# Kernel tuning notes

Measured on AMD Instinct MI355X. Metric: run time of the kernel, lower is better.

Reference implementation:

```python
import jax, jax.numpy as jnp
import numpy as np

N = 100000
E = 1600000
IN_FEATS = 256
HIDDEN = 128
CLASSES = 40

def _glorot(key, fan_in, fan_out):
    lim = float(np.sqrt(6.0 / (fan_in + fan_out)))
    return jax.random.uniform(key, (fan_in, fan_out), jnp.float32, -lim, lim)

def setup_inputs() -> dict:
    key = jax.random.key(0)
    ks = jax.random.split(key, 8)
    x = jax.random.normal(ks[0], (N, IN_FEATS), jnp.float32)
    src = jax.random.randint(ks[1], (E,), 0, N, jnp.int32)
    dst = jax.random.randint(ks[2], (E,), 0, N, jnp.int32)
    W0 = _glorot(ks[3], IN_FEATS, HIDDEN)
    b0 = jnp.zeros((HIDDEN,), jnp.float32)
    W1 = _glorot(ks[4], HIDDEN, HIDDEN)
    b1 = jnp.zeros((HIDDEN,), jnp.float32)
    Wc = _glorot(ks[5], HIDDEN, CLASSES)
    bc = jnp.zeros((CLASSES,), jnp.float32)
    return {"x": x, "src": src, "dst": dst, "W0": W0, "b0": b0,
            "W1": W1, "b1": b1, "Wc": Wc, "bc": bc}

def _degree_norms(src, dst, n):
    ones = jnp.ones(src.shape[0], jnp.float32)
    out_deg = jax.ops.segment_sum(ones, src, num_segments=n)
    in_deg = jax.ops.segment_sum(ones, dst, num_segments=n)
    c_src = jax.lax.rsqrt(jnp.maximum(out_deg, 1.0))  # D_out^{-1/2}
    c_dst = jax.lax.rsqrt(jnp.maximum(in_deg, 1.0))   # D_in^{-1/2}
    return c_src, c_dst

def _graph_conv(h, src, dst, c_src, c_dst, W, b, n):
    # transform first (cheaper when widths shrink), math-equivalent to DGL norm='both'
    h = h @ W
    h = h * c_src[:, None]
    agg = jax.ops.segment_sum(h[src], dst, num_segments=n)  # spmm gather/scatter
    return agg * c_dst[:, None] + b

def reference(x, src, dst, W0, b0, W1, b1, Wc, bc):
    n = x.shape[0]
    c_src, c_dst = _degree_norms(src, dst, n)
    h = _graph_conv(x, src, dst, c_src, c_dst, W0, b0, n)
    h = jax.nn.relu(h)  # dropout is identity at eval
    h = _graph_conv(h, src, dst, c_src, c_dst, W1, b1, n)
    logits = jax.nn.relu(h) @ Wc + bc
    return (h, logits)
```

## Files before the change

kernel.cpp:

```cpp
#include <hip/hip_runtime.h>
#include <cstdint>
#include <cstddef>


#define NPB 128
#define BSHIFT 7
#define NBLK_E 256

typedef __attribute__((ext_vector_type(8))) short short8;
typedef __attribute__((ext_vector_type(4))) float f32x4;

static __device__ __forceinline__ float4 ld4(const float* p) { return *(const float4*)p; }

static __device__ __forceinline__ float bf2f(unsigned int u) {
  union { unsigned int i; float f; } x; x.i = u << 16; return x.f;
}
static __device__ __forceinline__ unsigned int f2bf(float f) {
  union { float f; unsigned int i; } x; x.f = f;
  unsigned int r = x.i + 0x7fff + ((x.i >> 16) & 1);
  return r >> 16;
}

__global__ __launch_bounds__(256) void prep_weights(const float* __restrict__ W0,
                                                    const float* __restrict__ W1,
                                                    ushort* __restrict__ W0t,
                                                    ushort* __restrict__ W1t) {
  int t = blockIdx.x * 256 + threadIdx.x;
  if (t < 128 * 256) {
    int nn = t >> 8, kk = t & 255;
    W0t[nn * 256 + kk] = (ushort)f2bf(W0[kk * 128 + nn]);
  }
  if (t < 128 * 128) {
    int nn = t >> 7, kk = t & 127;
    W1t[nn * 128 + kk] = (ushort)f2bf(W1[kk * 128 + nn]);
  }
}

__global__ __launch_bounds__(256) void bucket_hist(const int* __restrict__ src,
                                                   const int* __restrict__ dst,
                                                   int* __restrict__ bhD, int* __restrict__ bhS,
                                                   int E, int nbk, int ept) {
  __shared__ int hD[1024], hS[1024];
  int t = threadIdx.x;
  for (int i = t; i < nbk; i += 256) { hD[i] = 0; hS[i] = 0; }
  __syncthreads();
  int base = blockIdx.x * 256 * ept + t;
  for (int j = 0; j < ept; j++) {
    int e = base + j * 256;
    if (e < E) {
      atomicAdd(&hD[dst[e] >> BSHIFT], 1);
      atomicAdd(&hS[src[e] >> BSHIFT], 1);
    }
  }
  __syncthreads();
  for (int i = t; i < nbk; i += 256) {
    bhD[(size_t)blockIdx.x * nbk + i] = hD[i];
    bhS[(size_t)blockIdx.x * nbk + i] = hS[i];
  }
}

__global__ __launch_bounds__(256) void bucket_scan_blocks(int* __restrict__ bhD,
                                                          int* __restrict__ bhS,
                                                          int* __restrict__ totD,
                                                          int* __restrict__ totS, int nbk) {
  __shared__ int lds[256];
  int b = blockIdx.x, t = threadIdx.x;
  int v = bhD[(size_t)t * nbk + b];
  lds[t] = v;
  __syncthreads();
  for (int off = 1; off < 256; off <<= 1) {
    int u = (t >= off) ? lds[t - off] : 0;
    __syncthreads();
    lds[t] += u;
    __syncthreads();
  }
  bhD[(size_t)t * nbk + b] = lds[t] - v;
  if (t == 255) totD[b] = lds[255];
  __syncthreads();
  int w = bhS[(size_t)t * nbk + b];
  lds[t] = w;
  __syncthreads();
  for (int off = 1; off < 256; off <<= 1) {
    int u = (t >= off) ? lds[t - off] : 0;
    __syncthreads();
    lds[t] += u;
    __syncthreads();
  }
  bhS[(size_t)t * nbk + b] = lds[t] - w;
  if (t == 255) totS[b] = lds[255];
}

__global__ __launch_bounds__(1024) void bucket_base(const int* __restrict__ totD,
                                                    const int* __restrict__ totS,
                                                    int* __restrict__ baseD,
                                                    int* __restrict__ baseS, int nbk) {
  __shared__ int lds[1024];
  int t = threadIdx.x;
  int v = (t < nbk) ? totD[t] : 0;
  lds[t] = v;
  __syncthreads();
  for (int off = 1; off < 1024; off <<= 1) {
    int u = (t >= off) ? lds[t - off] : 0;
    __syncthreads();
    lds[t] += u;
    __syncthreads();
  }
  if (t < nbk) baseD[t] = lds[t] - v;
  if (t == 1023) baseD[nbk] = lds[1023];
  __syncthreads();
  int w = (t < nbk) ? totS[t] : 0;
  lds[t] = w;
  __syncthreads();
  for (int off = 1; off < 1024; off <<= 1) {
    int u = (t >= off) ? lds[t - off] : 0;
    __syncthreads();
    lds[t] += u;
    __syncthreads();
  }
  if (t < nbk) baseS[t] = lds[t] - w;
  if (t == 1023) baseS[nbk] = lds[1023];
}

__global__ __launch_bounds__(256) void bucket_scatter(
    const int* __restrict__ src, const int* __restrict__ dst,
    const int* __restrict__ bhD, const int* __restrict__ bhS,
    const int* __restrict__ baseD, const int* __restrict__ baseS,
    unsigned int* __restrict__ ebufD, uint8_t* __restrict__ ebufS,
    int E, int nbk, int ept) {
  __shared__ int cD[1024], cS[1024];
  int k = blockIdx.x, t = threadIdx.x;
  for (int i = t; i < nbk; i += 256) {
    cD[i] = baseD[i] + bhD[(size_t)k * nbk + i];
    cS[i] = baseS[i] + bhS[(size_t)k * nbk + i];
  }
  __syncthreads();
  int base = k * 256 * ept + t;
  for (int j = 0; j < ept; j++) {
    int e = base + j * 256;
    if (e < E) {
      int s = src[e], d = dst[e];
      int pD = atomicAdd(&cD[d >> BSHIFT], 1);
      ebufD[pD] = ((unsigned int)(d & (NPB - 1)) << 17) | (unsigned int)s;
      int pS = atomicAdd(&cS[s >> BSHIFT], 1);
      ebufS[pS] = (uint8_t)(s & (NPB - 1));
    }
  }
}

__global__ __launch_bounds__(256) void csr_build(const unsigned int* __restrict__ ebufD,
                                                 const int* __restrict__ baseD,
                                                 int* __restrict__ row_start,
                                                 int* __restrict__ csr, int n, int nbk) {
  __shared__ int cnt[NPB], sc[NPB], cur[NPB];
  int b = blockIdx.x, t = threadIdx.x;
  if (t < NPB) cnt[t] = 0;
  __syncthreads();
  int s0 = baseD[b], s1 = baseD[b + 1];
  for (int i = s0 + t; i < s1; i += 256) atomicAdd(&cnt[ebufD[i] >> 17], 1);
  __syncthreads();
  int c = (t < NPB) ? cnt[t] : 0;
  if (t < NPB) sc[t] = c;
  __syncthreads();
  for (int off = 1; off < NPB; off <<= 1) {
    int u = (t < NPB && t >= off) ? sc[t - off] : 0;
    __syncthreads();
    if (t < NPB) sc[t] += u;
    __syncthreads();
  }
  if (t < NPB) {
    int start = s0 + sc[t] - c;
    cur[t] = start;
    int node = b * NPB + t;
    if (node < n) row_start[node] = start;
  }
  if (b == 0 && t == 0) row_start[n] = baseD[nbk];
  __syncthreads();
  for (int i = s0 + t; i < s1; i += 256) {
    unsigned int w = ebufD[i];
    int p = atomicAdd(&cur[w >> 17], 1);
    csr[p] = (int)(w & 0x1FFFFu);
  }
}

__global__ __launch_bounds__(256) void outdeg_norm(const uint8_t* __restrict__ ebufS,
                                                   const int* __restrict__ baseS,
                                                   float* __restrict__ c_src, int n) {
  __shared__ int cnt[NPB];
  int b = blockIdx.x, t = threadIdx.x;
  if (t < NPB) cnt[t] = 0;
  __syncthreads();
  int s0 = baseS[b], s1 = baseS[b + 1];
  for (int i = s0 + t; i < s1; i += 256) atomicAdd(&cnt[ebufS[i]], 1);
  __syncthreads();
  int node = b * NPB + t;
  if (t < NPB && node < n) c_src[node] = rsqrtf(fmaxf((float)cnt[t], 1.0f));
}


__global__ __launch_bounds__(256) void gemm256_mfma(const float* __restrict__ x,
                                                    const ushort* __restrict__ W0t,
                                                    const float* __restrict__ c_src,
                                                    ushort* __restrict__ t0b, int n) {
  __shared__ alignas(16) ushort As[64 * 64];
  __shared__ alignas(16) ushort Bs[128 * 64];
  int tid = threadIdx.x;
  int row0 = blockIdx.x * 64;
  int lane = tid & 63;
  int w = tid >> 6;
  int l16 = lane & 15, hi = lane >> 4;
  f32x4 acc[8];
#pragma unroll
  for (int c = 0; c < 8; c++) acc[c] = (f32x4){0.f, 0.f, 0.f, 0.f};

  for (int kt = 0; kt < 256; kt += 64) {
    {
      int r = tid >> 2;
      int gr = row0 + r;
#pragma unroll
      for (int u = 0; u < 2; u++) {
        int c8 = (tid & 3) * 2 + u;
        float4 v0 = make_float4(0.f, 0.f, 0.f, 0.f), v1 = v0;
        if (gr < n) {
          v0 = ld4(&x[(size_t)gr * 256 + kt + c8 * 8]);
          v1 = ld4(&x[(size_t)gr * 256 + kt + c8 * 8 + 4]);
        }
        uint4 o;
        o.x = f2bf(v0.x) | (f2bf(v0.y) << 16);
        o.y = f2bf(v0.z) | (f2bf(v0.w) << 16);
        o.z = f2bf(v1.x) | (f2bf(v1.y) << 16);
        o.w = f2bf(v1.z) | (f2bf(v1.w) << 16);
        *(uint4*)&As[r * 64 + (c8 ^ (r & 7)) * 8] = o;
      }
    }
    {
      int r = tid >> 1;
#pragma unroll
      for (int u = 0; u < 4; u++) {
        int c8 = (tid & 1) * 4 + u;
        uint4 o = *(const uint4*)&W0t[(size_t)r * 256 + kt + c8 * 8];
        *(uint4*)&Bs[r * 64 + (c8 ^ (r & 7)) * 8] = o;
      }
    }
    __syncthreads();
#pragma unroll
    for (int ks = 0; ks < 2; ks++) {
      int ar = w * 16 + l16;
      int ac = ks * 4 + hi;
      short8 a = *(const short8*)&As[ar * 64 + (ac ^ (ar & 7)) * 8];
#pragma unroll
      for (int c = 0; c < 8; c++) {
        int br = c * 16 + l16;
        short8 b = *(const short8*)&Bs[br * 64 + (ac ^ (br & 7)) * 8];
        acc[c] = __builtin_amdgcn_mfma_f32_16x16x32_bf16(a, b, acc[c], 0, 0, 0);
      }
    }
    __syncthreads();
  }
  float cs[4];
#pragma unroll
  for (int r = 0; r < 4; r++) {
    int gm = row0 + w * 16 + hi * 4 + r;
    cs[r] = (gm < n) ? c_src[gm] : 0.f;
  }
#pragma unroll
  for (int c = 0; c < 8; c++)
#pragma unroll
    for (int r = 0; r < 4; r++) {
      int gm = row0 + w * 16 + hi * 4 + r;
      if (gm < n) t0b[(size_t)gm * 128 + c * 16 + l16] = (ushort)f2bf(acc[c][r] * cs[r]);
    }
}

__global__ __launch_bounds__(256) void gemm128_mfma(const ushort* __restrict__ A,
                                                    const ushort* __restrict__ W1t,
                                                    const float* __restrict__ c_src,
                                                    ushort* __restrict__ Y, int n) {
  __shared__ alignas(16) ushort As[64 * 64];
  __shared__ alignas(16) ushort Bs[128 * 64];
  int tid = threadIdx.x;
  int row0 = blockIdx.x * 64;
  int lane = tid & 63;
  int w = tid >> 6;
  int l16 = lane & 15, hi = lane >> 4;
  f32x4 acc[8];
#pragma unroll
  for (int c = 0; c < 8; c++) acc[c] = (f32x4){0.f, 0.f, 0.f, 0.f};

  for (int kt = 0; kt < 128; kt += 64) {
    {
      int r = tid >> 2;
      int gr = row0 + r;
#pragma unroll
      for (int u = 0; u < 2; u++) {
        int c8 = (tid & 3) * 2 + u;
        uint4 o = make_uint4(0u, 0u, 0u, 0u);
        if (gr < n) o = *(const uint4*)&A[(size_t)gr * 128 + kt + c8 * 8];
        *(uint4*)&As[r * 64 + (c8 ^ (r & 7)) * 8] = o;
      }
    }
    {
      int r = tid >> 1;
#pragma unroll
      for (int u = 0; u < 4; u++) {
        int c8 = (tid & 1) * 4 + u;
        uint4 o = *(const uint4*)&W1t[(size_t)r * 128 + kt + c8 * 8];
        *(uint4*)&Bs[r * 64 + (c8 ^ (r & 7)) * 8] = o;
      }
    }
    __syncthreads();
#pragma unroll
    for (int ks = 0; ks < 2; ks++) {
      int ar = w * 16 + l16;
      int ac = ks * 4 + hi;
      short8 a = *(const short8*)&As[ar * 64 + (ac ^ (ar & 7)) * 8];
#pragma unroll
      for (int c = 0; c < 8; c++) {
        int br = c * 16 + l16;
        short8 b = *(const short8*)&Bs[br * 64 + (ac ^ (br & 7)) * 8];
        acc[c] = __builtin_amdgcn_mfma_f32_16x16x32_bf16(a, b, acc[c], 0, 0, 0);
      }
    }
    __syncthreads();
  }
  float cs[4];
#pragma unroll
  for (int r = 0; r < 4; r++) {
    int gm = row0 + w * 16 + hi * 4 + r;
    cs[r] = (gm < n) ? c_src[gm] : 0.f;
  }
#pragma unroll
  for (int c = 0; c < 8; c++)
#pragma unroll
    for (int r = 0; r < 4; r++) {
      int gm = row0 + w * 16 + hi * 4 + r;
      if (gm < n) Y[(size_t)gm * 128 + c * 16 + l16] = (ushort)f2bf(acc[c][r] * cs[r]);
    }
}

template <bool RELU, bool OUT_BF16>
__global__ __launch_bounds__(256) void agg_kernel(const ushort* __restrict__ T,
                                                  const int* __restrict__ row_start,
                                                  const int* __restrict__ csr_src,
                                                  const float* __restrict__ bias,
                                                  void* __restrict__ out, int n) {
  int lane = threadIdx.x & 63;
  int gw = (blockIdx.x * 256 + threadIdx.x) >> 6;
  int nw = gridDim.x * 4;
  float bx = bias[lane * 2], by = bias[lane * 2 + 1];
  for (int node = gw; node < n; node += nw) {
    int e0 = row_start[node], e1 = row_start[node + 1];
    float ax = 0.f, ay = 0.f;
    for (int eb = e0; eb < e1; eb += 64) {
      int rem = e1 - eb;
      int cnt = rem < 64 ? rem : 64;
      int msrc = (lane < rem) ? csr_src[eb + lane] : 0;
      int j = 0;
      for (; j + 7 < cnt; j += 8) {
        unsigned int w[8];
#pragma unroll
        for (int u = 0; u < 8; u++) {
          int s = __shfl(msrc, j + u);
          w[u] = *(const unsigned int*)&T[(size_t)s * 128 + lane * 2];
        }
#pragma unroll
        for (int u = 0; u < 8; u++) {
          ax += bf2f(w[u] & 0xffff);
          ay += bf2f(w[u] >> 16);
        }
      }
      for (; j + 1 < cnt; j += 2) {
        int s0 = __shfl(msrc, j), s1 = __shfl(msrc, j + 1);
        unsigned int w0 = *(const unsigned int*)&T[(size_t)s0 * 128 + lane * 2];
        unsigned int w1 = *(const unsigned int*)&T[(size_t)s1 * 128 + lane * 2];
        ax += bf2f(w0 & 0xffff) + bf2f(w1 & 0xffff);
        ay += bf2f(w0 >> 16) + bf2f(w1 >> 16);
      }
      if (j < cnt) {
        int s0 = __shfl(msrc, j);
        unsigned int w0 = *(const unsigned int*)&T[(size_t)s0 * 128 + lane * 2];
        ax += bf2f(w0 & 0xffff);
        ay += bf2f(w0 >> 16);
      }
    }
    float cd = rsqrtf(fmaxf((float)(e1 - e0), 1.0f));
    float rx = fmaf(ax, cd, bx);
    float ry = fmaf(ay, cd, by);
    if (RELU) { rx = fmaxf(rx, 0.f); ry = fmaxf(ry, 0.f); }
    if (OUT_BF16) {
      ((unsigned int*)out)[(size_t)node * 64 + lane] = f2bf(rx) | (f2bf(ry) << 16);
    } else {
      float2 r2; r2.x = rx; r2.y = ry;
      ((float2*)out)[(size_t)node * 64 + lane] = r2;
    }
  }
}

__global__ __launch_bounds__(256) void logits_kernel(const float* __restrict__ H,
                                                     const float* __restrict__ Wc,
                                                     const float* __restrict__ bc,
                                                     float* __restrict__ out, int n) {
  __shared__ float Wl[128 * 40];
  for (int i = threadIdx.x; i < 128 * 40; i += 256) Wl[i] = Wc[i];
  __syncthreads();
  int rl = threadIdx.x >> 3;
  int cg = threadIdx.x & 7;
  int r = blockIdx.x * 32 + rl;
  if (r >= n) return;
  float acc[5] = {0.f, 0.f, 0.f, 0.f, 0.f};
  const float* hr = &H[(size_t)r * 128];
  for (int k = 0; k < 128; k++) {
    float v = fmaxf(hr[k], 0.f);
#pragma unroll
    for (int j = 0; j < 5; j++) acc[j] = fmaf(v, Wl[k * 40 + cg * 5 + j], acc[j]);
  }
#pragma unroll
  for (int j = 0; j < 5; j++) out[(size_t)r * 40 + cg * 5 + j] = acc[j] + bc[cg * 5 + j];
}

extern "C" void kernel_launch(void* const* d_in, const int* in_sizes, int n_in,
                              void* d_out, int out_size, void* d_ws, size_t ws_size,
                              hipStream_t stream) {
  const float* x = (const float*)d_in[0];
  const int* src = (const int*)d_in[1];
  const int* dst = (const int*)d_in[2];
  const float* W0 = (const float*)d_in[3];
  const float* b0 = (const float*)d_in[4];
  const float* W1 = (const float*)d_in[5];
  const float* b1 = (const float*)d_in[6];
  const float* Wc = (const float*)d_in[7];
  const float* bc = (const float*)d_in[8];
  const int n = in_sizes[0] / 256;
  const int E = in_sizes[1];
  const int nbk = (n + NPB - 1) >> BSHIFT;
  const int ept = (E + NBLK_E * 256 - 1) / (NBLK_E * 256);

  char* wsp = (char*)d_ws;
  auto alloc = [&](size_t bytes) -> char* {
    char* p = wsp;
    wsp += (bytes + 255) & ~(size_t)255;
    return p;
  };
  ushort* t0b = (ushort*)alloc((size_t)n * 128 * sizeof(ushort));
  ushort* h1b = (ushort*)alloc((size_t)n * 128 * sizeof(ushort));
  float* c_src = (float*)alloc((size_t)n * sizeof(float));
  ushort* W0t = (ushort*)alloc((size_t)128 * 256 * sizeof(ushort));
  ushort* W1t = (ushort*)alloc((size_t)128 * 128 * sizeof(ushort));
  int* bhD = (int*)alloc((size_t)NBLK_E * nbk * sizeof(int));
  int* bhS = (int*)alloc((size_t)NBLK_E * nbk * sizeof(int));
  int* totD = (int*)alloc((size_t)nbk * sizeof(int));
  int* totS = (int*)alloc((size_t)nbk * sizeof(int));
  int* baseD = (int*)alloc((size_t)(nbk + 1) * sizeof(int));
  int* baseS = (int*)alloc((size_t)(nbk + 1) * sizeof(int));
  unsigned int* ebufD = (unsigned int*)alloc((size_t)E * sizeof(unsigned int));
  uint8_t* ebufS = (uint8_t*)alloc((size_t)E);
  int* row_start = (int*)alloc((size_t)(n + 1) * sizeof(int));
  int* csr = (int*)alloc((size_t)E * sizeof(int));

  float* h_out = (float*)d_out;
  float* logits = h_out + (size_t)n * 128;

  prep_weights<<<128, 256, 0, stream>>>(W0, W1, W0t, W1t);

  bucket_hist<<<NBLK_E, 256, 0, stream>>>(src, dst, bhD, bhS, E, nbk, ept);
  bucket_scan_blocks<<<nbk, 256, 0, stream>>>(bhD, bhS, totD, totS, nbk);
  bucket_base<<<1, 1024, 0, stream>>>(totD, totS, baseD, baseS, nbk);
  bucket_scatter<<<NBLK_E, 256, 0, stream>>>(src, dst, bhD, bhS, baseD, baseS,
                                             ebufD, ebufS, E, nbk, ept);
  csr_build<<<nbk, 256, 0, stream>>>(ebufD, baseD, row_start, csr, n, nbk);
  outdeg_norm<<<nbk, 256, 0, stream>>>(ebufS, baseS, c_src, n);

  gemm256_mfma<<<(n + 63) / 64, 256, 0, stream>>>(x, W0t, c_src, t0b, n);
  agg_kernel<true, true><<<2048, 256, 0, stream>>>(
      t0b, row_start, csr, b0, (void*)h1b, n);
  gemm128_mfma<<<(n + 63) / 64, 256, 0, stream>>>(h1b, W1t, c_src, t0b, n);
  agg_kernel<false, false><<<2048, 256, 0, stream>>>(
      t0b, row_start, csr, b1, (void*)h_out, n);
  logits_kernel<<<(n + 31) / 32, 256, 0, stream>>>(h_out, Wc, bc, logits, n);
}
```

Measured before the change: 460.9 us.

## Fuse graph preprocessing into one persistent kernel overlapped with first GEMM

Merges the six CSR-building and degree kernels into one persistent kernel that uses global atomic-counter grid barriers between phases. Extra blocks in the same launch run the first-layer GEMM at the same time, so the GEMM no longer waits on c_src. The source-degree scaling moves into the first aggregation as a per-edge multiply, and the out-degree count is merged into the CSR build pass. This removes launch overhead and serialisation, at the cost of spin-wait grid barriers that deadlock unless all 256 preprocessing blocks are co-resident, plus extra per-edge c_src gathers in aggregation.

```diff
diff --git a/kernel.cpp b/kernel.cpp
--- a/kernel.cpp
+++ b/kernel.cpp
@@ -5,7 +5,8 @@
 
 #define NPB 128
 #define BSHIFT 7
-#define NBLK_E 256
+#define NBLD 256
+#define GEMM_G 1536
 
 typedef __attribute__((ext_vector_type(8))) short short8;
 typedef __attribute__((ext_vector_type(4))) float f32x4;
@@ -21,11 +22,24 @@
   return r >> 16;
 }
 
+static __device__ __forceinline__ void bbar(int* ctr, int expected) {
+  __syncthreads();
+  if (threadIdx.x == 0) {
+    __threadfence();
+    atomicAdd(ctr, 1);
+    while (atomicAdd(ctr, 0) < expected) __builtin_amdgcn_s_sleep(8);
+  }
+  __syncthreads();
+  __threadfence();
+}
+
 __global__ __launch_bounds__(256) void prep_weights(const float* __restrict__ W0,
                                                     const float* __restrict__ W1,
                                                     ushort* __restrict__ W0t,
-                                                    ushort* __restrict__ W1t) {
+                                                    ushort* __restrict__ W1t,
+                                                    int* __restrict__ bar) {
   int t = blockIdx.x * 256 + threadIdx.x;
+  if (t < 8) bar[t] = 0;
   if (t < 128 * 256) {
     int nn = t >> 8, kk = t & 255;
     W0t[nn * 256 + kk] = (ushort)f2bf(W0[kk * 128 + nn]);
@@ -36,239 +50,215 @@
   }
 }
 
-__global__ __launch_bounds__(256) void bucket_hist(const int* __restrict__ src,
-                                                   const int* __restrict__ dst,
-                                                   int* __restrict__ bhD, int* __restrict__ bhS,
-                                                   int E, int nbk, int ept) {
-  __shared__ int hD[1024], hS[1024];
-  int t = threadIdx.x;
-  for (int i = t; i < nbk; i += 256) { hD[i] = 0; hS[i] = 0; }
-  __syncthreads();
-  int base = blockIdx.x * 256 * ept + t;
+__global__ __launch_bounds__(256) void mega(
+    const int* src, const int* dst,
+    int* bhD, int* bhS, int* totD, int* totS, int* baseD, int* baseS,
+    unsigned int* ebufD, uint8_t* ebufS, int* row_start, int* csr, float* c_src,
+    const float* x, const ushort* W0t, ushort* t0b,
+    int* bar, int n, int E, int nbk, int ept, int ngemm) {
+  __shared__ alignas(16) union {
+    struct { ushort As[64 * 64]; ushort Bs[128 * 64]; } g;
+    struct { int a[1024]; int b[1024]; } h;
+    int scan[1024];
+    struct { int cnt[NPB]; int sc[NPB]; int cur[NPB]; int cntS[NPB]; } cb;
+  } sm;
+  int bid = blockIdx.x, t = threadIdx.x;
+
+  if (bid >= NBLD) {
+    int lane = t & 63;
+    int w = t >> 6;
+    int l16 = lane & 15, hi = lane >> 4;
+    for (int tile = bid - NBLD; tile < ngemm; tile += GEMM_G - NBLD) {
+      int row0 = tile * 64;
+      f32x4 acc[8];
+#pragma unroll
+      for (int c = 0; c < 8; c++) acc[c] = (f32x4){0.f, 0.f, 0.f, 0.f};
+      for (int kt = 0; kt < 256; kt += 64) {
+        {
+          int r = t >> 2;
+          int gr = row0 + r;
+#pragma unroll
+          for (int u = 0; u < 2; u++) {
+            int c8 = (t & 3) * 2 + u;
+            float4 v0 = make_float4(0.f, 0.f, 0.f, 0.f), v1 = v0;
+            if (gr < n) {
+              v0 = ld4(&x[(size_t)gr * 256 + kt + c8 * 8]);
+              v1 = ld4(&x[(size_t)gr * 256 + kt + c8 * 8 + 4]);
+            }
+            uint4 o;
+            o.x = f2bf(v0.x) | (f2bf(v0.y) << 16);
+            o.y = f2bf(v0.z) | (f2bf(v0.w) << 16);
+            o.z = f2bf(v1.x) | (f2bf(v1.y) << 16);
+            o.w = f2bf(v1.z) | (f2bf(v1.w) << 16);
+            *(uint4*)&sm.g.As[r * 64 + (c8 ^ (r & 7)) * 8] = o;
+          }
+        }
+        {
+          int r = t >> 1;
+#pragma unroll
+          for (int u = 0; u < 4; u++) {
+            int c8 = (t & 1) * 4 + u;
+            uint4 o = *(const uint4*)&W0t[(size_t)r * 256 + kt + c8 * 8];
+            *(uint4*)&sm.g.Bs[r * 64 + (c8 ^ (r & 7)) * 8] = o;
+          }
+        }
+        __syncthreads();
+#pragma unroll
+        for (int ks = 0; ks < 2; ks++) {
+          int ar = w * 16 + l16;
+          int ac = ks * 4 + hi;
+          short8 a = *(const short8*)&sm.g.As[ar * 64 + (ac ^ (ar & 7)) * 8];
+#pragma unroll
+          for (int c = 0; c < 8; c++) {
+            int br = c * 16 + l16;
+            short8 b = *(const short8*)&sm.g.Bs[br * 64 + (ac ^ (br & 7)) * 8];
+            acc[c] = __builtin_amdgcn_mfma_f32_16x16x32_bf16(a, b, acc[c], 0, 0, 0);
+          }
+        }
+        __syncthreads();
+      }
+#pragma unroll
+      for (int c = 0; c < 8; c++)
+#pragma unroll
+        for (int r = 0; r < 4; r++) {
+          int gm = row0 + w * 16 + hi * 4 + r;
+          if (gm < n) t0b[(size_t)gm * 128 + c * 16 + l16] = (ushort)f2bf(acc[c][r]);
+        }
+    }
+    return;
+  }
+
+  int base0 = bid * 256 * ept + t;
+  for (int i = t; i < nbk; i += 256) { sm.h.a[i] = 0; sm.h.b[i] = 0; }
+  __syncthreads();
   for (int j = 0; j < ept; j++) {
-    int e = base + j * 256;
+    int e = base0 + j * 256;
     if (e < E) {
-      atomicAdd(&hD[dst[e] >> BSHIFT], 1);
-      atomicAdd(&hS[src[e] >> BSHIFT], 1);
+      atomicAdd(&sm.h.a[dst[e] >> BSHIFT], 1);
+      atomicAdd(&sm.h.b[src[e] >> BSHIFT], 1);
     }
   }
   __syncthreads();
   for (int i = t; i < nbk; i += 256) {
-    bhD[(size_t)blockIdx.x * nbk + i] = hD[i];
-    bhS[(size_t)blockIdx.x * nbk + i] = hS[i];
-  }
-}
-
-__global__ __launch_bounds__(256) void bucket_scan_blocks(int* __restrict__ bhD,
-                                                          int* __restrict__ bhS,
-                                                          int* __restrict__ totD,
-                                                          int* __restrict__ totS, int nbk) {
-  __shared__ int lds[256];
-  int b = blockIdx.x, t = threadIdx.x;
-  int v = bhD[(size_t)t * nbk + b];
-  lds[t] = v;
-  __syncthreads();
-  for (int off = 1; off < 256; off <<= 1) {
-    int u = (t >= off) ? lds[t - off] : 0;
-    __syncthreads();
-    lds[t] += u;
-    __syncthreads();
-  }
-  bhD[(size_t)t * nbk + b] = lds[t] - v;
-  if (t == 255) totD[b] = lds[255];
-  __syncthreads();
-  int w = bhS[(size_t)t * nbk + b];
-  lds[t] = w;
-  __syncthreads();
-  for (int off = 1; off < 256; off <<= 1) {
-    int u = (t >= off) ? lds[t - off] : 0;
-    __syncthreads();
-    lds[t] += u;
-    __syncthreads();
-  }
-  bhS[(size_t)t * nbk + b] = lds[t] - w;
-  if (t == 255) totS[b] = lds[255];
-}
-
-__global__ __launch_bounds__(1024) void bucket_base(const int* __restrict__ totD,
-                                                    const int* __restrict__ totS,
-                                                    int* __restrict__ baseD,
-                                                    int* __restrict__ baseS, int nbk) {
-  __shared__ int lds[1024];
-  int t = threadIdx.x;
-  int v = (t < nbk) ? totD[t] : 0;
-  lds[t] = v;
-  __syncthreads();
-  for (int off = 1; off < 1024; off <<= 1) {
-    int u = (t >= off) ? lds[t - off] : 0;
-    __syncthreads();
-    lds[t] += u;
-    __syncthreads();
-  }
-  if (t < nbk) baseD[t] = lds[t] - v;
-  if (t == 1023) baseD[nbk] = lds[1023];
-  __syncthreads();
-  int w = (t < nbk) ? totS[t] : 0;
-  lds[t] = w;
-  __syncthreads();
-  for (int off = 1; off < 1024; off <<= 1) {
-    int u = (t >= off) ? lds[t - off] : 0;
-    __syncthreads();
-    lds[t] += u;
-    __syncthreads();
-  }
-  if (t < nbk) baseS[t] = lds[t] - w;
-  if (t == 1023) baseS[nbk] = lds[1023];
-}
-
-__global__ __launch_bounds__(256) void bucket_scatter(
-    const int* __restrict__ src, const int* __restrict__ dst,
-    const int* __restrict__ bhD, const int* __restrict__ bhS,
-    const int* __restrict__ baseD, const int* __restrict__ baseS,
-    unsigned int* __restrict__ ebufD, uint8_t* __restrict__ ebufS,
-    int E, int nbk, int ept) {
-  __shared__ int cD[1024], cS[1024];
-  int k = blockIdx.x, t = threadIdx.x;
+    bhD[(size_t)bid * nbk + i] = sm.h.a[i];
+    bhS[(size_t)bid * nbk + i] = sm.h.b[i];
+  }
+  bbar(&bar[0], NBLD);
+
+  for (int c = bid; c < nbk; c += NBLD) {
+    int v = bhD[(size_t)t * nbk + c];
+    sm.scan[t] = v;
+    __syncthreads();
+    for (int off = 1; off < 256; off <<= 1) {
+      int u = (t >= off) ? sm.scan[t - off] : 0;
+      __syncthreads();
+      sm.scan[t] += u;
+      __syncthreads();
+    }
+    bhD[(size_t)t * nbk + c] = sm.scan[t] - v;
+    if (t == 255) totD[c] = sm.scan[255];
+    __syncthreads();
+    int w2 = bhS[(size_t)t * nbk + c];
+    sm.scan[t] = w2;
+    __syncthreads();
+    for (int off = 1; off < 256; off <<= 1) {
+      int u = (t >= off) ? sm.scan[t - off] : 0;
+      __syncthreads();
+      sm.scan[t] += u;
+      __syncthreads();
+    }
+    bhS[(size_t)t * nbk + c] = sm.scan[t] - w2;
+    if (t == 255) totS[c] = sm.scan[255];
+    __syncthreads();
+  }
+  bbar(&bar[1], NBLD);
+
+  if (bid == 0) {
+#pragma unroll
+    for (int side = 0; side < 2; side++) {
+      const int* tot = side ? totS : totD;
+      int* bse = side ? baseS : baseD;
+      int v[4];
+      int s = 0;
+#pragma unroll
+      for (int j = 0; j < 4; j++) {
+        int idx = t * 4 + j;
+        v[j] = (idx < nbk) ? tot[idx] : 0;
+        s += v[j];
+      }
+      sm.scan[t] = s;
+      __syncthreads();
+      for (int off = 1; off < 256; off <<= 1) {
+        int u = (t >= off) ? sm.scan[t - off] : 0;
+        __syncthreads();
+        sm.scan[t] += u;
+        __syncthreads();
+      }
+      int run = sm.scan[t] - s;
+#pragma unroll
+      for (int j = 0; j < 4; j++) {
+        int idx = t * 4 + j;
+        if (idx < nbk) bse[idx] = run;
+        run += v[j];
+      }
+      if (t == 255) bse[nbk] = run;
+      __syncthreads();
+    }
+  }
+  bbar(&bar[2], NBLD);
+
   for (int i = t; i < nbk; i += 256) {
-    cD[i] = baseD[i] + bhD[(size_t)k * nbk + i];
-    cS[i] = baseS[i] + bhS[(size_t)k * nbk + i];
-  }
-  __syncthreads();
-  int base = k * 256 * ept + t;
+    sm.h.a[i] = baseD[i] + bhD[(size_t)bid * nbk + i];
+    sm.h.b[i] = baseS[i] + bhS[(size_t)bid * nbk + i];
+  }
+  __syncthreads();
   for (int j = 0; j < ept; j++) {
-    int e = base + j * 256;
+    int e = base0 + j * 256;
     if (e < E) {
       int s = src[e], d = dst[e];
-      int pD = atomicAdd(&cD[d >> BSHIFT], 1);
+      int pD = atomicAdd(&sm.h.a[d >> BSHIFT], 1);
       ebufD[pD] = ((unsigned int)(d & (NPB - 1)) << 17) | (unsigned int)s;
-      int pS = atomicAdd(&cS[s >> BSHIFT], 1);
+      int pS = atomicAdd(&sm.h.b[s >> BSHIFT], 1);
       ebufS[pS] = (uint8_t)(s & (NPB - 1));
     }
   }
-}
-
-__global__ __launch_bounds__(256) void csr_build(const unsigned int* __restrict__ ebufD,
-                                                 const int* __restrict__ baseD,
-                                                 int* __restrict__ row_start,
-                                                 int* __restrict__ csr, int n, int nbk) {
-  __shared__ int cnt[NPB], sc[NPB], cur[NPB];
-  int b = blockIdx.x, t = threadIdx.x;
-  if (t < NPB) cnt[t] = 0;
-  __syncthreads();
-  int s0 = baseD[b], s1 = baseD[b + 1];
-  for (int i = s0 + t; i < s1; i += 256) atomicAdd(&cnt[ebufD[i] >> 17], 1);
-  __syncthreads();
-  int c = (t < NPB) ? cnt[t] : 0;
-  if (t < NPB) sc[t] = c;
-  __syncthreads();
-  for (int off = 1; off < NPB; off <<= 1) {
-    int u = (t < NPB && t >= off) ? sc[t - off] : 0;
-    __syncthreads();
-    if (t < NPB) sc[t] += u;
-    __syncthreads();
-  }
-  if (t < NPB) {
-    int start = s0 + sc[t] - c;
-    cur[t] = start;
-    int node = b * NPB + t;
-    if (node < n) row_start[node] = start;
-  }
-  if (b == 0 && t == 0) row_start[n] = baseD[nbk];
-  __syncthreads();
-  for (int i = s0 + t; i < s1; i += 256) {
-    unsigned int w = ebufD[i];
-    int p = atomicAdd(&cur[w >> 17], 1);
-    csr[p] = (int)(w & 0x1FFFFu);
-  }
-}
-
-__global__ __launch_bounds__(256) void outdeg_norm(const uint8_t* __restrict__ ebufS,
-                                                   const int* __restrict__ baseS,
-                                                   float* __restrict__ c_src, int n) {
-  __shared__ int cnt[NPB];
-  int b = blockIdx.x, t = threadIdx.x;
-  if (t < NPB) cnt[t] = 0;
-  __syncthreads();
-  int s0 = baseS[b], s1 = baseS[b + 1];
-  for (int i = s0 + t; i < s1; i += 256) atomicAdd(&cnt[ebufS[i]], 1);
-  __syncthreads();
-  int node = b * NPB + t;
-  if (t < NPB && node < n) c_src[node] = rsqrtf(fmaxf((float)cnt[t], 1.0f));
-}
-
-
-__global__ __launch_bounds__(256) void gemm256_mfma(const float* __restrict__ x,
-                                                    const ushort* __restrict__ W0t,
-                                                    const float* __restrict__ c_src,
-                                                    ushort* __restrict__ t0b, int n) {
-  __shared__ alignas(16) ushort As[64 * 64];
-  __shared__ alignas(16) ushort Bs[128 * 64];
-  int tid = threadIdx.x;
-  int row0 = blockIdx.x * 64;
-  int lane = tid & 63;
-  int w = tid >> 6;
-  int l16 = lane & 15, hi = lane >> 4;
-  f32x4 acc[8];
-#pragma unroll
-  for (int c = 0; c < 8; c++) acc[c] = (f32x4){0.f, 0.f, 0.f, 0.f};
-
-  for (int kt = 0; kt < 256; kt += 64) {
-    {
-      int r = tid >> 2;
-      int gr = row0 + r;
-#pragma unroll
-      for (int u = 0; u < 2; u++) {
-        int c8 = (tid & 3) * 2 + u;
-        float4 v0 = make_float4(0.f, 0.f, 0.f, 0.f), v1 = v0;
-        if (gr < n) {
-          v0 = ld4(&x[(size_t)gr * 256 + kt + c8 * 8]);
-          v1 = ld4(&x[(size_t)gr * 256 + kt + c8 * 8 + 4]);
-        }
-        uint4 o;
-        o.x = f2bf(v0.x) | (f2bf(v0.y) << 16);
-        o.y = f2bf(v0.z) | (f2bf(v0.w) << 16);
-        o.z = f2bf(v1.x) | (f2bf(v1.y) << 16);
-        o.w = f2bf(v1.z) | (f2bf(v1.w) << 16);
-        *(uint4*)&As[r * 64 + (c8 ^ (r & 7)) * 8] = o;
-      }
-    }
-    {
-      int r = tid >> 1;
-#pragma unroll
-      for (int u = 0; u < 4; u++) {
-        int c8 = (tid & 1) * 4 + u;
-        uint4 o = *(const uint4*)&W0t[(size_t)r * 256 + kt + c8 * 8];
-        *(uint4*)&Bs[r * 64 + (c8 ^ (r & 7)) * 8] = o;
-      }
-    }
-    __syncthreads();
-#pragma unroll
-    for (int ks = 0; ks < 2; ks++) {
-      int ar = w * 16 + l16;
-      int ac = ks * 4 + hi;
-      short8 a = *(const short8*)&As[ar * 64 + (ac ^ (ar & 7)) * 8];
-#pragma unroll
-      for (int c = 0; c < 8; c++) {
-        int br = c * 16 + l16;
-        short8 b = *(const short8*)&Bs[br * 64 + (ac ^ (br & 7)) * 8];
-        acc[c] = __builtin_amdgcn_mfma_f32_16x16x32_bf16(a, b, acc[c], 0, 0, 0);
-      }
-    }
-    __syncthreads();
-  }
-  float cs[4];
-#pragma unroll
-  for (int r = 0; r < 4; r++) {
-    int gm = row0 + w * 16 + hi * 4 + r;
-    cs[r] = (gm < n) ? c_src[gm] : 0.f;
-  }
-#pragma unroll
-  for (int c = 0; c < 8; c++)
-#pragma unroll
-    for (int r = 0; r < 4; r++) {
-      int gm = row0 + w * 16 + hi * 4 + r;
-      if (gm < n) t0b[(size_t)gm * 128 + c * 16 + l16] = (ushort)f2bf(acc[c][r] * cs[r]);
-    }
+  bbar(&bar[3], NBLD);
+
+  for (int bk = bid; bk < nbk; bk += NBLD) {
+    if (t < NPB) { sm.cb.cnt[t] = 0; sm.cb.cntS[t] = 0; }
+    __syncthreads();
+    int s0 = baseD[bk], s1 = baseD[bk + 1];
+    for (int i = s0 + t; i < s1; i += 256) atomicAdd(&sm.cb.cnt[ebufD[i] >> 17], 1);
+    int u0 = baseS[bk], u1 = baseS[bk + 1];
+    for (int i = u0 + t; i < u1; i += 256) atomicAdd(&sm.cb.cntS[ebufS[i]], 1);
+    __syncthreads();
+    int c = (t < NPB) ? sm.cb.cnt[t] : 0;
+    if (t < NPB) sm.cb.sc[t] = c;
+    __syncthreads();
+    for (int off = 1; off < NPB; off <<= 1) {
+      int u = (t < NPB && t >= off) ? sm.cb.sc[t - off] : 0;
+      __syncthreads();
+      if (t < NPB) sm.cb.sc[t] += u;
+      __syncthreads();
+    }
+    if (t < NPB) {
+      int start = s0 + sm.cb.sc[t] - c;
+      sm.cb.cur[t] = start;
+      int node = bk * NPB + t;
+      if (node < n) {
+        row_start[node] = start;
+        c_src[node] = rsqrtf(fmaxf((float)sm.cb.cntS[t], 1.0f));
+      }
+    }
+    if (bk == 0 && t == 0) row_start[n] = baseD[nbk];
+    __syncthreads();
+    for (int i = s0 + t; i < s1; i += 256) {
+      unsigned int wv = ebufD[i];
+      int p = atomicAdd(&sm.cb.cur[wv >> 17], 1);
+      csr[p] = (int)(wv & 0x1FFFFu);
+    }
+    __syncthreads();
+  }
 }
 
 __global__ __launch_bounds__(256) void gemm128_mfma(const ushort* __restrict__ A,
@@ -337,10 +327,11 @@
     }
 }
 
-template <bool RELU, bool OUT_BF16>
+template <bool RELU, bool SCALE, bool OUT_BF16>
 __global__ __launch_bounds__(256) void agg_kernel(const ushort* __restrict__ T,
                                                   const int* __restrict__ row_start,
                                                   const int* __restrict__ csr_src,
+                                                  const float* __restrict__ c_src,
                                                   const float* __restrict__ bias,
                                                   void* __restrict__ out, int n) {
   int lane = threadIdx.x & 63;
@@ -354,32 +345,40 @@
       int rem = e1 - eb;
       int cnt = rem < 64 ? rem : 64;
       int msrc = (lane < rem) ? csr_src[eb + lane] : 0;
+      float mcs = 1.f;
+      if (SCALE) mcs = (lane < rem) ? c_src[msrc] : 0.f;
       int j = 0;
       for (; j + 7 < cnt; j += 8) {
         unsigned int w[8];
+        float cs8[8];
 #pragma unroll
         for (int u = 0; u < 8; u++) {
           int s = __shfl(msrc, j + u);
+          if (SCALE) cs8[u] = __shfl(mcs, j + u);
           w[u] = *(const unsigned int*)&T[(size_t)s * 128 + lane * 2];
         }
 #pragma unroll
         for (int u = 0; u < 8; u++) {
-          ax += bf2f(w[u] & 0xffff);
-          ay += bf2f(w[u] >> 16);
-        }
-      }
-      for (; j + 1 < cnt; j += 2) {
-        int s0 = __shfl(msrc, j), s1 = __shfl(msrc, j + 1);
-        unsigned int w0 = *(const unsigned int*)&T[(size_t)s0 * 128 + lane * 2];
-        unsigned int w1 = *(const unsigned int*)&T[(size_t)s1 * 128 + lane * 2];
-        ax += bf2f(w0 & 0xffff) + bf2f(w1 & 0xffff);
-        ay += bf2f(w0 >> 16) + bf2f(w1 >> 16);
-      }
-      if (j < cnt) {
-        int s0 = __shfl(msrc, j);
-        unsigned int w0 = *(const unsigned int*)&T[(size_t)s0 * 128 + lane * 2];
-        ax += bf2f(w0 & 0xffff);
-        ay += bf2f(w0 >> 16);
+          if (SCALE) {
+            ax = fmaf(bf2f(w[u] & 0xffff), cs8[u], ax);
+            ay = fmaf(bf2f(w[u] >> 16), cs8[u], ay);
+          } else {
+            ax += bf2f(w[u] & 0xffff);
+            ay += bf2f(w[u] >> 16);
+          }
+        }
+      }
+      for (; j < cnt; j++) {
+        int s = __shfl(msrc, j);
+        float cs = SCALE ? __shfl(mcs, j) : 1.f;
+        unsigned int w0 = *(const unsigned int*)&T[(size_t)s * 128 + lane * 2];
+        if (SCALE) {
+          ax = fmaf(bf2f(w0 & 0xffff), cs, ax);
+          ay = fmaf(bf2f(w0 >> 16), cs, ay);
+        } else {
+          ax += bf2f(w0 & 0xffff);
+          ay += bf2f(w0 >> 16);
+        }
       }
     }
     float cd = rsqrtf(fmaxf((float)(e1 - e0), 1.0f));
@@ -432,7 +431,7 @@
   const int n = in_sizes[0] / 256;
   const int E = in_sizes[1];
   const int nbk = (n + NPB - 1) >> BSHIFT;
-  const int ept = (E + NBLK_E * 256 - 1) / (NBLK_E * 256);
+  const int ept = (E + NBLD * 256 - 1) / (NBLD * 256);
 
   char* wsp = (char*)d_ws;
   auto alloc = [&](size_t bytes) -> char* {
@@ -445,8 +444,8 @@
   float* c_src = (float*)alloc((size_t)n * sizeof(float));
   ushort* W0t = (ushort*)alloc((size_t)128 * 256 * sizeof(ushort));
   ushort* W1t = (ushort*)alloc((size_t)128 * 128 * sizeof(ushort));
-  int* bhD = (int*)alloc((size_t)NBLK_E * nbk * sizeof(int));
-  int* bhS = (int*)alloc((size_t)NBLK_E * nbk * sizeof(int));
+  int* bhD = (int*)alloc((size_t)NBLD * nbk * sizeof(int));
+  int* bhS = (int*)alloc((size_t)NBLD * nbk * sizeof(int));
   int* totD = (int*)alloc((size_t)nbk * sizeof(int));
   int* totS = (int*)alloc((size_t)nbk * sizeof(int));
   int* baseD = (int*)alloc((size_t)(nbk + 1) * sizeof(int));
@@ -455,25 +454,21 @@
   uint8_t* ebufS = (uint8_t*)alloc((size_t)E);
   int* row_start = (int*)alloc((size_t)(n + 1) * sizeof(int));
   int* csr = (int*)alloc((size_t)E * sizeof(int));
+  int* bar = (int*)alloc((size_t)8 * sizeof(int));
 
   float* h_out = (float*)d_out;
   float* logits = h_out + (size_t)n * 128;
 
-  prep_weights<<<128, 256, 0, stream>>>(W0, W1, W0t, W1t);
-
-  bucket_hist<<<NBLK_E, 256, 0, stream>>>(src, dst, bhD, bhS, E, nbk, ept);
-  bucket_scan_blocks<<<nbk, 256, 0, stream>>>(bhD, bhS, totD, totS, nbk);
-  bucket_base<<<1, 1024, 0, stream>>>(totD, totS, baseD, baseS, nbk);
-  bucket_scatter<<<NBLK_E, 256, 0, stream>>>(src, dst, bhD, bhS, baseD, baseS,
-                                             ebufD, ebufS, E, nbk, ept);
-  csr_build<<<nbk, 256, 0, stream>>>(ebufD, baseD, row_start, csr, n, nbk);
-  outdeg_norm<<<nbk, 256, 0, stream>>>(ebufS, baseS, c_src, n);
-
-  gemm256_mfma<<<(n + 63) / 64, 256, 0, stream>>>(x, W0t, c_src, t0b, n);
-  agg_kernel<true, true><<<2048, 256, 0, stream>>>(
-      t0b, row_start, csr, b0, (void*)h1b, n);
+  const int ngemm = (n + 63) / 64;
+
+  prep_weights<<<128, 256, 0, stream>>>(W0, W1, W0t, W1t, bar);
+  mega<<<GEMM_G, 256, 0, stream>>>(src, dst, bhD, bhS, totD, totS, baseD, baseS,
+                                   ebufD, ebufS, row_start, csr, c_src,
+                                   x, W0t, t0b, bar, n, E, nbk, ept, ngemm);
+  agg_kernel<true, true, true><<<2048, 256, 0, stream>>>(
+      t0b, row_start, csr, c_src, b0, (void*)h1b, n);
   gemm128_mfma<<<(n + 63) / 64, 256, 0, stream>>>(h1b, W1t, c_src, t0b, n);
-  agg_kernel<false, false><<<2048, 256, 0, stream>>>(
-      t0b, row_start, csr, b1, (void*)h_out, n);
+  agg_kernel<false, false, false><<<2048, 256, 0, stream>>>(
+      t0b, row_start, csr, c_src, b1, (void*)h_out, n);
   logits_kernel<<<(n + 31) / 32, 256, 0, stream>>>(h_out, Wc, bc, logits, n);
 }
```

Result: slower. 586.7 us (+27.3%).

## Locally sort edges in LDS before bucket scatter and merge CSR with out-degree

Applied to the files above, without the earlier changes.

The bucket scatter kernel now sorts each chunk of edges by bucket in shared memory, then writes them to global memory in bucket order, so global stores are grouped into contiguous runs instead of being scattered one by one. The chunk size becomes a fixed compile-time value (25 edges per thread), which changes the block count of the histogram and scan. The CSR build and out-degree normalisation kernels are merged into one launch. The cost is a second histogram pass, extra LDS use that lowers occupancy, and a binary search per element during the write-out.

```diff
diff --git a/kernel.cpp b/kernel.cpp
--- a/kernel.cpp
+++ b/kernel.cpp
@@ -5,7 +5,8 @@
 
 #define NPB 128
 #define BSHIFT 7
-#define NBLK_E 256
+#define EPT3 25
+#define CHUNK (EPT3 * 256)
 
 typedef __attribute__((ext_vector_type(8))) short short8;
 typedef __attribute__((ext_vector_type(4))) float f32x4;
@@ -39,13 +40,13 @@
 __global__ __launch_bounds__(256) void bucket_hist(const int* __restrict__ src,
                                                    const int* __restrict__ dst,
                                                    int* __restrict__ bhD, int* __restrict__ bhS,
-                                                   int E, int nbk, int ept) {
+                                                   int E, int nbk) {
   __shared__ int hD[1024], hS[1024];
   int t = threadIdx.x;
   for (int i = t; i < nbk; i += 256) { hD[i] = 0; hS[i] = 0; }
   __syncthreads();
-  int base = blockIdx.x * 256 * ept + t;
-  for (int j = 0; j < ept; j++) {
+  int base = blockIdx.x * CHUNK + t;
+  for (int j = 0; j < EPT3; j++) {
     int e = base + j * 256;
     if (e < E) {
       atomicAdd(&hD[dst[e] >> BSHIFT], 1);
@@ -62,10 +63,11 @@
 __global__ __launch_bounds__(256) void bucket_scan_blocks(int* __restrict__ bhD,
                                                           int* __restrict__ bhS,
                                                           int* __restrict__ totD,
-                                                          int* __restrict__ totS, int nbk) {
+                                                          int* __restrict__ totS,
+                                                          int nbk, int nblk) {
   __shared__ int lds[256];
   int b = blockIdx.x, t = threadIdx.x;
-  int v = bhD[(size_t)t * nbk + b];
+  int v = (t < nblk) ? bhD[(size_t)t * nbk + b] : 0;
   lds[t] = v;
   __syncthreads();
   for (int off = 1; off < 256; off <<= 1) {
@@ -74,10 +76,10 @@
     lds[t] += u;
     __syncthreads();
   }
-  bhD[(size_t)t * nbk + b] = lds[t] - v;
+  if (t < nblk) bhD[(size_t)t * nbk + b] = lds[t] - v;
   if (t == 255) totD[b] = lds[255];
   __syncthreads();
-  int w = bhS[(size_t)t * nbk + b];
+  int w = (t < nblk) ? bhS[(size_t)t * nbk + b] : 0;
   lds[t] = w;
   __syncthreads();
   for (int off = 1; off < 256; off <<= 1) {
@@ -86,7 +88,7 @@
     lds[t] += u;
     __syncthreads();
   }
-  bhS[(size_t)t * nbk + b] = lds[t] - w;
+  if (t < nblk) bhS[(size_t)t * nbk + b] = lds[t] - w;
   if (t == 255) totS[b] = lds[255];
 }
 
@@ -121,42 +123,105 @@
   if (t == 1023) baseS[nbk] = lds[1023];
 }
 
-__global__ __launch_bounds__(256) void bucket_scatter(
+__global__ __launch_bounds__(256) void sort_scatter(
     const int* __restrict__ src, const int* __restrict__ dst,
     const int* __restrict__ bhD, const int* __restrict__ bhS,
     const int* __restrict__ baseD, const int* __restrict__ baseS,
     unsigned int* __restrict__ ebufD, uint8_t* __restrict__ ebufS,
-    int E, int nbk, int ept) {
-  __shared__ int cD[1024], cS[1024];
-  int k = blockIdx.x, t = threadIdx.x;
+    int E, int nbk) {
+  __shared__ int binD[1024], binS[1024];
+  __shared__ int bbD[1024], bbS[1024];
+  __shared__ int scanT[256];
+  __shared__ unsigned int sortD[CHUNK];
+  __shared__ uint8_t sortS[CHUNK];
+  int bid = blockIdx.x, t = threadIdx.x;
+  int base0 = bid * CHUNK;
+  int cc = min(CHUNK, E - base0);
+  for (int i = t; i < 1024; i += 256) { binD[i] = 0; binS[i] = 0; }
+  __syncthreads();
+  for (int j = 0; j < EPT3; j++) {
+    int e = base0 + j * 256 + t;
+    if (e < E) {
+      atomicAdd(&binD[dst[e] >> BSHIFT], 1);
+      atomicAdd(&binS[src[e] >> BSHIFT], 1);
+    }
+  }
+  __syncthreads();
+  {
+    int v[4]; int s = 0;
+#pragma unroll
+    for (int j = 0; j < 4; j++) { v[j] = binD[t * 4 + j]; s += v[j]; }
+    scanT[t] = s;
+    __syncthreads();
+    for (int off = 1; off < 256; off <<= 1) {
+      int u = (t >= off) ? scanT[t - off] : 0;
+      __syncthreads();
+      scanT[t] += u;
+      __syncthreads();
+    }
+    int run = scanT[t] - s;
+#pragma unroll
+    for (int j = 0; j < 4; j++) { binD[t * 4 + j] = run; run += v[j]; }
+    __syncthreads();
+    s = 0;
+#pragma unroll
+    for (int j = 0; j < 4; j++) { v[j] = binS[t * 4 + j]; s += v[j]; }
+    scanT[t] = s;
+    __syncthreads();
+    for (int off = 1; off < 256; off <<= 1) {
+      int u = (t >= off) ? scanT[t - off] : 0;
+      __syncthreads();
+      scanT[t] += u;
+      __syncthreads();
+    }
+    run = scanT[t] - s;
+#pragma unroll
+    for (int j = 0; j < 4; j++) { binS[t * 4 + j] = run; run += v[j]; }
+    __syncthreads();
+  }
   for (int i = t; i < nbk; i += 256) {
-    cD[i] = baseD[i] + bhD[(size_t)k * nbk + i];
-    cS[i] = baseS[i] + bhS[(size_t)k * nbk + i];
-  }
-  __syncthreads();
-  int base = k * 256 * ept + t;
-  for (int j = 0; j < ept; j++) {
-    int e = base + j * 256;
+    bbD[i] = baseD[i] + bhD[(size_t)bid * nbk + i] - binD[i];
+    bbS[i] = baseS[i] + bhS[(size_t)bid * nbk + i] - binS[i];
+  }
+  __syncthreads();
+  for (int j = 0; j < EPT3; j++) {
+    int e = base0 + j * 256 + t;
     if (e < E) {
       int s = src[e], d = dst[e];
-      int pD = atomicAdd(&cD[d >> BSHIFT], 1);
-      ebufD[pD] = ((unsigned int)(d & (NPB - 1)) << 17) | (unsigned int)s;
-      int pS = atomicAdd(&cS[s >> BSHIFT], 1);
-      ebufS[pS] = (uint8_t)(s & (NPB - 1));
-    }
-  }
-}
-
-__global__ __launch_bounds__(256) void csr_build(const unsigned int* __restrict__ ebufD,
-                                                 const int* __restrict__ baseD,
-                                                 int* __restrict__ row_start,
-                                                 int* __restrict__ csr, int n, int nbk) {
-  __shared__ int cnt[NPB], sc[NPB], cur[NPB];
+      int pD = atomicAdd(&binD[d >> BSHIFT], 1);
+      sortD[pD] = ((unsigned int)(d & (NPB - 1)) << 17) | (unsigned int)s;
+      int pS = atomicAdd(&binS[s >> BSHIFT], 1);
+      sortS[pS] = (uint8_t)(s & (NPB - 1));
+    }
+  }
+  __syncthreads();
+  for (int i = t; i < cc; i += 256) {
+    int b = 0;
+#pragma unroll
+    for (int step = 512; step; step >>= 1)
+      if (b + step <= nbk && binD[b + step - 1] <= i) b += step;
+    ebufD[bbD[b] + i] = sortD[i];
+    int b2 = 0;
+#pragma unroll
+    for (int step = 512; step; step >>= 1)
+      if (b2 + step <= nbk && binS[b2 + step - 1] <= i) b2 += step;
+    ebufS[bbS[b2] + i] = sortS[i];
+  }
+}
+
+__global__ __launch_bounds__(256) void csr_outdeg(
+    const unsigned int* __restrict__ ebufD, const uint8_t* __restrict__ ebufS,
+    const int* __restrict__ baseD, const int* __restrict__ baseS,
+    int* __restrict__ row_start, int* __restrict__ csr,
+    float* __restrict__ c_src, int n, int nbk) {
+  __shared__ int cnt[NPB], sc[NPB], cur[NPB], cntS[NPB];
   int b = blockIdx.x, t = threadIdx.x;
-  if (t < NPB) cnt[t] = 0;
+  if (t < NPB) { cnt[t] = 0; cntS[t] = 0; }
   __syncthreads();
   int s0 = baseD[b], s1 = baseD[b + 1];
   for (int i = s0 + t; i < s1; i += 256) atomicAdd(&cnt[ebufD[i] >> 17], 1);
+  int u0 = baseS[b], u1 = baseS[b + 1];
+  for (int i = u0 + t; i < u1; i += 256) atomicAdd(&cntS[ebufS[i]], 1);
   __syncthreads();
   int c = (t < NPB) ? cnt[t] : 0;
   if (t < NPB) sc[t] = c;
@@ -171,29 +236,18 @@
     int start = s0 + sc[t] - c;
     cur[t] = start;
     int node = b * NPB + t;
-    if (node < n) row_start[node] = start;
+    if (node < n) {
+      row_start[node] = start;
+      c_src[node] = rsqrtf(fmaxf((float)cntS[t], 1.0f));
+    }
   }
   if (b == 0 && t == 0) row_start[n] = baseD[nbk];
   __syncthreads();
   for (int i = s0 + t; i < s1; i += 256) {
-    unsigned int w = ebufD[i];
-    int p = atomicAdd(&cur[w >> 17], 1);
-    csr[p] = (int)(w & 0x1FFFFu);
-  }
-}
-
-__global__ __launch_bounds__(256) void outdeg_norm(const uint8_t* __restrict__ ebufS,
-                                                   const int* __restrict__ baseS,
-                                                   float* __restrict__ c_src, int n) {
-  __shared__ int cnt[NPB];
-  int b = blockIdx.x, t = threadIdx.x;
-  if (t < NPB) cnt[t] = 0;
-  __syncthreads();
-  int s0 = baseS[b], s1 = baseS[b + 1];
-  for (int i = s0 + t; i < s1; i += 256) atomicAdd(&cnt[ebufS[i]], 1);
-  __syncthreads();
-  int node = b * NPB + t;
-  if (t < NPB && node < n) c_src[node] = rsqrtf(fmaxf((float)cnt[t], 1.0f));
+    unsigned int wv = ebufD[i];
+    int p = atomicAdd(&cur[wv >> 17], 1);
+    csr[p] = (int)(wv & 0x1FFFFu);
+  }
 }
 
 
@@ -432,7 +486,7 @@
   const int n = in_sizes[0] / 256;
   const int E = in_sizes[1];
   const int nbk = (n + NPB - 1) >> BSHIFT;
-  const int ept = (E + NBLK_E * 256 - 1) / (NBLK_E * 256);
+  const int nblk = (E + CHUNK - 1) / CHUNK;
 
   char* wsp = (char*)d_ws;
   auto alloc = [&](size_t bytes) -> char* {
@@ -445,8 +499,8 @@
   float* c_src = (float*)alloc((size_t)n * sizeof(float));
   ushort* W0t = (ushort*)alloc((size_t)128 * 256 * sizeof(ushort));
   ushort* W1t = (ushort*)alloc((size_t)128 * 128 * sizeof(ushort));
-  int* bhD = (int*)alloc((size_t)NBLK_E * nbk * sizeof(int));
-  int* bhS = (int*)alloc((size_t)NBLK_E * nbk * sizeof(int));
+  int* bhD = (int*)alloc((size_t)nblk * nbk * sizeof(int));
+  int* bhS = (int*)alloc((size_t)nblk * nbk * sizeof(int));
   int* totD = (int*)alloc((size_t)nbk * sizeof(int));
   int* totS = (int*)alloc((size_t)nbk * sizeof(int));
   int* baseD = (int*)alloc((size_t)(nbk + 1) * sizeof(int));
@@ -460,15 +514,13 @@
   float* logits = h_out + (size_t)n * 128;
 
   prep_weights<<<128, 256, 0, stream>>>(W0, W1, W0t, W1t);
-
-  bucket_hist<<<NBLK_E, 256, 0, stream>>>(src, dst, bhD, bhS, E, nbk, ept);
-  bucket_scan_blocks<<<nbk, 256, 0, stream>>>(bhD, bhS, totD, totS, nbk);
+  bucket_hist<<<nblk, 256, 0, stream>>>(src, dst, bhD, bhS, E, nbk);
+  bucket_scan_blocks<<<nbk, 256, 0, stream>>>(bhD, bhS, totD, totS, nbk, nblk);
   bucket_base<<<1, 1024, 0, stream>>>(totD, totS, baseD, baseS, nbk);
-  bucket_scatter<<<NBLK_E, 256, 0, stream>>>(src, dst, bhD, bhS, baseD, baseS,
-                                             ebufD, ebufS, E, nbk, ept);
-  csr_build<<<nbk, 256, 0, stream>>>(ebufD, baseD, row_start, csr, n, nbk);
-  outdeg_norm<<<nbk, 256, 0, stream>>>(ebufS, baseS, c_src, n);
-
+  sort_scatter<<<nblk, 256, 0, stream>>>(src, dst, bhD, bhS, baseD, baseS,
+                                         ebufD, ebufS, E, nbk);
+  csr_outdeg<<<nbk, 256, 0, stream>>>(ebufD, ebufS, baseD, baseS,
+                                      row_start, csr, c_src, n, nbk);
   gemm256_mfma<<<(n + 63) / 64, 256, 0, stream>>>(x, W0t, c_src, t0b, n);
   agg_kernel<true, true><<<2048, 256, 0, stream>>>(
       t0b, row_start, csr, b0, (void*)h1b, n);
```

After: 467.1 us. No clear change (+1.3%).
